# Optimization experiments

Measured on AMD Instinct MI355X. Metric: run time of the kernel, lower is better.

The kernel has to match this reference:

```python
import jax, jax.numpy as jnp
import numpy as np

N_NODES = 200000
N_EDGES = 3200000
N_GRAPHS = 2000
N_MAX = 256   # max nodes per graph for dense batching (mean ~100)
K = 30        # SortAggregation k


def setup_inputs() -> dict:
    key = jax.random.key(0)
    ks = jax.random.split(key, 12)
    x = jax.random.normal(ks[0], (N_NODES, 128), jnp.float32)
    edge_index = jax.random.randint(ks[1], (2, N_EDGES), 0, N_NODES, dtype=jnp.int32)
    batch = jnp.sort(jax.random.randint(ks[2], (N_NODES,), 0, N_GRAPHS, dtype=jnp.int32))
    def lin(k, i, o):
        return (jax.random.normal(k, (i, o), jnp.float32) / np.sqrt(i)).astype(jnp.float32)
    return {
        'x': x, 'edge_index': edge_index, 'batch': batch,
        'W1': lin(ks[3], 128, 32), 'b1': jnp.zeros(32, jnp.float32),
        'W2': lin(ks[4], 32, 32),  'b2': jnp.zeros(32, jnp.float32),
        'W3': lin(ks[5], 32, 32),  'b3': jnp.zeros(32, jnp.float32),
        'W4': lin(ks[6], 32, 1),   'b4': jnp.zeros(1, jnp.float32),
        'cw5': (jax.random.normal(ks[7], (16, 1, 97), jnp.float32) / np.sqrt(97)).astype(jnp.float32),
        'cb5': jnp.zeros(16, jnp.float32),
        'cw6': (jax.random.normal(ks[8], (32, 16, 5), jnp.float32) / np.sqrt(80)).astype(jnp.float32),
        'cb6': jnp.zeros(32, jnp.float32),
        'fw1': lin(ks[9], 352, 128), 'fb1': jnp.zeros(128, jnp.float32),
        'fw2': lin(ks[10], 128, 10), 'fb2': jnp.zeros(10, jnp.float32),
    }


def _gcn_conv(h, W, b, src, dst, emask):
    # PyG GCNConv: remove self-loops handled via emask (weight 0), then add
    # self-loops weight 1; symmetric normalization D^{-1/2}(A+I)D^{-1/2} X W + b
    deg = jax.ops.segment_sum(emask, dst, num_segments=N_NODES) + 1.0  # + self loop
    dis = jax.lax.rsqrt(deg)  # deg >= 1 always, no inf
    norm = dis[src] * dis[dst] * emask  # [E]
    hw = h @ W                          # [N, out]
    agg = jax.ops.segment_sum(hw[src] * norm[:, None], dst, num_segments=N_NODES)
    agg = agg + hw * (dis * dis)[:, None]  # self-loop message
    return agg + b


def _sort_pool(x, batch):
    # PyG SortAggregation(k): dense-batch with fill = min-1, sort each graph by
    # last feature channel (descending), keep top-k rows, zero out padding, flatten.
    N, D = x.shape
    ones = jnp.ones((N,), jnp.int32)
    counts = jax.ops.segment_sum(ones, batch, num_segments=N_GRAPHS)
    offsets = jnp.concatenate([jnp.zeros((1,), jnp.int32), jnp.cumsum(counts)[:-1]])
    pos = jnp.arange(N, dtype=jnp.int32) - offsets[batch]  # batch is sorted
    fill = x.min() - 1.0
    dense = jnp.full((N_GRAPHS, N_MAX, D), fill, x.dtype).at[batch, pos].set(x)
    perm = jnp.argsort(-dense[:, :, -1], axis=1)            # descending by last channel
    dense = jnp.take_along_axis(dense, perm[:, :, None], axis=1)[:, :K]  # [G, K, D]
    dense = jnp.where(dense == fill, 0.0, dense)
    return dense.reshape(N_GRAPHS, K * D)


def _conv1d(x, w, b, stride):
    y = jax.lax.conv_general_dilated(x, w, window_strides=(stride,), padding='VALID',
                                     dimension_numbers=('NCH', 'OIH', 'NCH'))
    return y + b[None, :, None]


def reference(x, edge_index, batch, W1, b1, W2, b2, W3, b3, W4, b4,
              cw5, cb5, cw6, cb6, fw1, fb1, fw2, fb2):
    src, dst = edge_index[0], edge_index[1]
    emask = (src != dst).astype(x.dtype)  # remove_self_loops

    x1 = jnp.tanh(_gcn_conv(x,  W1, b1, src, dst, emask))
    x2 = jnp.tanh(_gcn_conv(x1, W2, b2, src, dst, emask))
    x3 = jnp.tanh(_gcn_conv(x2, W3, b3, src, dst, emask))
    x4 = jnp.tanh(_gcn_conv(x3, W4, b4, src, dst, emask))
    h = jnp.concatenate([x1, x2, x3, x4], axis=-1)  # [N, 97]

    p = _sort_pool(h, batch)                 # [G, 30*97]
    p = p[:, None, :]                        # [G, 1, 2910]
    p = jax.nn.relu(_conv1d(p, cw5, cb5, 97))  # [G, 16, 30]
    G = p.shape[0]
    p = p.reshape(G, 16, 15, 2).max(axis=-1)   # MaxPool1d(2,2) -> [G, 16, 15]
    p = jax.nn.relu(_conv1d(p, cw6, cb6, 1))   # [G, 32, 11]
    p = p.reshape(G, -1)                       # [G, 352]
    out = jax.nn.relu(p @ fw1 + fb1)           # dropout is identity at inference
    return jax.nn.log_softmax(out @ fw2 + fb2, axis=-1)
```

## Files before the change

### kernel.cpp

```cpp
#include <hip/hip_runtime.h>

#define N_NODESC 200000
#define N_EDGESC 3200000
#define N_GRAPHSC 2000
#define NMAXG 256
#define TOPK 30
#define DCAT 97
#define POOLW (TOPK*DCAT)
#define BUCKW 512
#define NBUCK ((N_NODESC+BUCKW-1)/BUCKW)
#define CAP 10240
#define PCHUNK 4096
#define NPBLK ((N_EDGESC+PCHUNK-1)/PCHUNK)

typedef int  iv4 __attribute__((ext_vector_type(4)));
typedef float fv4 __attribute__((ext_vector_type(4)));

__global__ __launch_bounds__(256) void k_binit(int* __restrict__ bcur){
  int i = blockIdx.x*256 + threadIdx.x;
  if (i < NBUCK) bcur[i] = i*CAP;
}

__global__ __launch_bounds__(256) void k_part(const int* __restrict__ src, const int* __restrict__ dst,
                                              int* __restrict__ bcur, unsigned* __restrict__ pairbuf){
  __shared__ int hcnt[NBUCK];
  __shared__ int hbase[NBUCK];
  int blk = blockIdx.x, t = threadIdx.x;
  int e0 = blk*PCHUNK;
  int e1 = e0 + PCHUNK; if (e1 > N_EDGESC) e1 = N_EDGESC;
  for (int i=t;i<NBUCK;i+=256) hcnt[i]=0;
  unsigned pk[16]; unsigned meta[16];
  __syncthreads();
  #pragma unroll
  for (int i=0;i<4;i++){
    int e = e0 + i*1024 + t*4;
    if (e < e1){
      iv4 d4 = __builtin_nontemporal_load((const iv4*)(dst+e));
      iv4 s4 = __builtin_nontemporal_load((const iv4*)(src+e));
      #pragma unroll
      for (int k=0;k<4;k++){
        int d = (k==0)?d4.x:(k==1)?d4.y:(k==2)?d4.z:d4.w;
        int s = (k==0)?s4.x:(k==1)?s4.y:(k==2)?s4.z:s4.w;
        if (s!=d){
          int bk = d>>9;
          int pl = atomicAdd(&hcnt[bk],1);
          pk[i*4+k]   = ((unsigned)(d&511)<<18)|(unsigned)s;
          meta[i*4+k] = ((unsigned)bk<<13)|(unsigned)pl;
        } else meta[i*4+k] = 0xFFFFFFFFu;
      }
    } else {
      #pragma unroll
      for (int k=0;k<4;k++) meta[i*4+k] = 0xFFFFFFFFu;
    }
  }
  __syncthreads();
  for (int i=t;i<NBUCK;i+=256){
    int c = hcnt[i];
    hbase[i] = c ? atomicAdd(&bcur[i],c) : 0;
  }
  __syncthreads();
  #pragma unroll
  for (int k=0;k<16;k++){
    unsigned m = meta[k];
    if (m != 0xFFFFFFFFu){
      int bk = (int)(m>>13);
      int pos = hbase[bk] + (int)(m & 0x1FFFu);
      if (pos < (bk+1)*CAP) pairbuf[pos] = pk[k];
    }
  }
}

__global__ __launch_bounds__(512) void k_bsort(const unsigned* __restrict__ pairbuf, const int* __restrict__ bcur,
                                               int* __restrict__ degc, int* __restrict__ offs,
                                               float* __restrict__ dis, int* __restrict__ csr){
  __shared__ int lcsr[CAP];
  __shared__ int lcnt[512];
  __shared__ int lofs[512];
  __shared__ int lcur[512];
  __shared__ int red[512];
  int b = blockIdx.x, t = threadIdx.x;
  int cnt_b = bcur[b] - b*CAP; if (cnt_b > CAP) cnt_b = CAP;
  int pv = 0;
  if (t < b){ int c = bcur[t]-t*CAP; if (c>CAP) c=CAP; pv = c; }
  red[t]=pv; __syncthreads();
  for (int off=256;off>0;off>>=1){ if (t<off) red[t]+=red[t+off]; __syncthreads(); }
  int base = red[0];
  const unsigned* pb = pairbuf + (size_t)b*CAP;
  lcnt[t]=0; __syncthreads();
  for (int i=t;i<cnt_b;i+=512) atomicAdd(&lcnt[pb[i]>>18],1);
  __syncthreads();
  lofs[t]=lcnt[t]; __syncthreads();
  for (int off=1;off<512;off<<=1){
    int u = (t>=off)? lofs[t-off] : 0;
    __syncthreads();
    lofs[t]+=u;
    __syncthreads();
  }
  int excl = lofs[t]-lcnt[t];
  int node = b*BUCKW + t;
  if (node < N_NODESC){
    degc[node] = lcnt[t];
    offs[node] = base + excl;
    dis[node]  = rsqrtf((float)lcnt[t] + 1.0f);
  }
  lcur[t]=excl;
  __syncthreads();
  for (int i=t;i<cnt_b;i+=512){
    unsigned v = pb[i];
    int p = atomicAdd(&lcur[v>>18],1);
    lcsr[p] = (int)(v & 0x3FFFFu);
  }
  __syncthreads();
  for (int i=t;i<cnt_b;i+=512) csr[base+i]=lcsr[i];
}

__global__ void k_bhist(const int* __restrict__ batch, int* __restrict__ gcount){
  int i = blockIdx.x*256 + threadIdx.x;
  if (i < N_NODESC) atomicAdd(&gcount[batch[i]],1);
}

__global__ __launch_bounds__(1024) void k_gscan(const int* __restrict__ gcount, int* __restrict__ goff){
  __shared__ int sm[1024];
  int t=threadIdx.x;
  int i0=2*t, i1=2*t+1;
  int v0 = (i0<N_GRAPHSC)? gcount[i0]:0;
  int v1 = (i1<N_GRAPHSC)? gcount[i1]:0;
  int s = v0+v1;
  sm[t]=s; __syncthreads();
  for (int off=1;off<1024;off<<=1){
    int u=(t>=off)? sm[t-off]:0;
    __syncthreads();
    sm[t]+=u;
    __syncthreads();
  }
  int excl = sm[t]-s;
  if (i0<N_GRAPHSC) goff[i0]=excl;
  if (i1<N_GRAPHSC) goff[i1]=excl+v0;
}

template<int KIN>
__global__ __launch_bounds__(256) void k_mm(const float* __restrict__ X, const float* __restrict__ W,
                                            const float* __restrict__ dis, float* __restrict__ out){
  __shared__ float xs[256*33];
  int r0 = blockIdx.x*256;
  int t = threadIdx.x;
  int r = r0 + t;
  float acc[32];
  #pragma unroll
  for (int f=0;f<32;f++) acc[f]=0.f;
  for (int kc=0; kc<KIN; kc+=32){
    __syncthreads();
    #pragma unroll
    for (int it=0; it<8; it++){
      int idx = it*256 + t;
      int row = idx>>3, c4 = idx&7;
      int gr = r0 + row;
      fv4 v = {0.f,0.f,0.f,0.f};
      if (gr < N_NODESC) v = __builtin_nontemporal_load((const fv4*)(X + (size_t)gr*KIN + kc + c4*4));
      int bofs = row*33 + c4*4;
      xs[bofs]=v.x; xs[bofs+1]=v.y; xs[bofs+2]=v.z; xs[bofs+3]=v.w;
    }
    __syncthreads();
    const float* w0 = W + kc*32;
    const float* xrow = xs + t*33;
    #pragma unroll
    for (int k=0;k<32;k++){
      float xv = xrow[k];
      #pragma unroll
      for (int f=0;f<32;f++) acc[f] = fmaf(xv, w0[k*32+f], acc[f]);
    }
  }
  if (r >= N_NODESC) return;
  float d = dis[r];
  float4* op = (float4*)(out + (size_t)r*32);
  #pragma unroll
  for (int f4=0;f4<8;f4++)
    op[f4] = make_float4(acc[4*f4]*d, acc[4*f4+1]*d, acc[4*f4+2]*d, acc[4*f4+3]*d);
}

__global__ void k_mm4(const float* __restrict__ X, const float* __restrict__ W, const float* __restrict__ dis, float* __restrict__ out){
  int r = blockIdx.x*256+threadIdx.x;
  if (r>=N_NODESC) return;
  const float4* xr = (const float4*)(X + (size_t)r*32);
  float acc=0.f;
  #pragma unroll
  for (int k4=0;k4<8;k4++){
    float4 xv = xr[k4];
    acc = fmaf(xv.x, W[k4*4+0], acc);
    acc = fmaf(xv.y, W[k4*4+1], acc);
    acc = fmaf(xv.z, W[k4*4+2], acc);
    acc = fmaf(xv.w, W[k4*4+3], acc);
  }
  out[r]=acc*dis[r];
}

__global__ __launch_bounds__(256) void k_agg(const float* __restrict__ hws, const int* __restrict__ csr,
                      const int* __restrict__ off, const int* __restrict__ cnt,
                      const float* __restrict__ dis, const float* __restrict__ bias,
                      float* __restrict__ out){
  int t = blockIdx.x*256 + threadIdx.x;
  int n = t>>5;
  if (n>=N_NODESC) return;
  int f = t&31;
  int beg = off[n], c = cnt[n];
  float a0=0.f,a1=0.f,a2=0.f,a3=0.f,a4=0.f,a5=0.f,a6=0.f,a7=0.f;
  for (int base=0; base<c; base+=32){
    int m = c-base; if (m>32) m=32;
    int idx = (f<m)? csr[beg+base+f] : 0;
    int j=0;
    for (; j+8<=m; j+=8){
      int s0=__shfl(idx,j,32),   s1=__shfl(idx,j+1,32),
          s2=__shfl(idx,j+2,32), s3=__shfl(idx,j+3,32),
          s4=__shfl(idx,j+4,32), s5=__shfl(idx,j+5,32),
          s6=__shfl(idx,j+6,32), s7=__shfl(idx,j+7,32);
      float v0=hws[(size_t)s0*32+f];
      float v1=hws[(size_t)s1*32+f];
      float v2=hws[(size_t)s2*32+f];
      float v3=hws[(size_t)s3*32+f];
      float v4=hws[(size_t)s4*32+f];
      float v5=hws[(size_t)s5*32+f];
      float v6=hws[(size_t)s6*32+f];
      float v7=hws[(size_t)s7*32+f];
      a0+=v0; a1+=v1; a2+=v2; a3+=v3; a4+=v4; a5+=v5; a6+=v6; a7+=v7;
    }
    for (; j+4<=m; j+=4){
      int s0=__shfl(idx,j,32), s1=__shfl(idx,j+1,32),
          s2=__shfl(idx,j+2,32), s3=__shfl(idx,j+3,32);
      float v0=hws[(size_t)s0*32+f];
      float v1=hws[(size_t)s1*32+f];
      float v2=hws[(size_t)s2*32+f];
      float v3=hws[(size_t)s3*32+f];
      a0+=v0; a1+=v1; a2+=v2; a3+=v3;
    }
    for (; j<m; j++){
      int s0=__shfl(idx,j,32);
      a0 += hws[(size_t)s0*32+f];
    }
  }
  float dn = dis[n];
  float sum = ((a0+a1)+(a2+a3)) + ((a4+a5)+(a6+a7));
  float v = dn*(sum+hws[(size_t)n*32+f]) + bias[f];
  out[(size_t)n*32+f] = tanhf(v);
}

__global__ void k_agg4(const float* __restrict__ hws4, const int* __restrict__ csr,
                       const int* __restrict__ off, const int* __restrict__ cnt,
                       const float* __restrict__ dis, const float* __restrict__ b4,
                       float* __restrict__ x4){
  int n = blockIdx.x*256+threadIdx.x;
  if (n>=N_NODESC) return;
  int beg=off[n], c=cnt[n];
  float a0=0.f,a1=0.f,a2=0.f,a3=0.f,a4=0.f,a5=0.f,a6=0.f,a7=0.f;
  int e=0;
  for (; e+8<=c; e+=8){
    int s0=csr[beg+e],   s1=csr[beg+e+1], s2=csr[beg+e+2], s3=csr[beg+e+3];
    int s4=csr[beg+e+4], s5=csr[beg+e+5], s6=csr[beg+e+6], s7=csr[beg+e+7];
    a0+=hws4[s0]; a1+=hws4[s1]; a2+=hws4[s2]; a3+=hws4[s3];
    a4+=hws4[s4]; a5+=hws4[s5]; a6+=hws4[s6]; a7+=hws4[s7];
  }
  for (; e<c; e++) a0+=hws4[csr[beg+e]];
  float dn=dis[n];
  float sum = ((a0+a1)+(a2+a3)) + ((a4+a5)+(a6+a7));
  x4[n] = tanhf(dn*(sum+hws4[n]) + b4[0]);
}

__global__ __launch_bounds__(256) void k_sortpool(const float* __restrict__ x1,const float* __restrict__ x2,const float* __restrict__ x3,const float* __restrict__ x4,
                           const int* __restrict__ gcount, const int* __restrict__ goff, float* __restrict__ pool){
  __shared__ float vals[NMAXG];
  __shared__ int sel[TOPK];
  int g = blockIdx.x;
  int start = goff[g];
  int cntg = gcount[g]; if (cntg>NMAXG) cntg=NMAXG;
  int t = threadIdx.x;
  float v = 0.f;
  if (t<cntg) v = x4[start+t];
  vals[t] = v;
  __syncthreads();
  if (t<cntg){
    int rank=0;
    for (int j=0;j<cntg;j++){
      float vj=vals[j];
      rank += (vj>v) || (vj==v && j<t);
    }
    if (rank<TOPK) sel[rank]=t;
  }
  __syncthreads();
  int nsel = cntg<TOPK?cntg:TOPK;
  float* pg = pool + (size_t)g*POOLW;
  for (int idx=t; idx<POOLW; idx+=256){
    int r = idx/DCAT, c = idx - r*DCAT;
    float val=0.f;
    if (r<nsel){
      int node = start + sel[r];
      if (c<32) val = x1[(size_t)node*32+c];
      else if (c<64) val = x2[(size_t)node*32+(c-32)];
      else if (c<96) val = x3[(size_t)node*32+(c-64)];
      else val = x4[node];
    }
    pg[idx]=val;
  }
}

__global__ __launch_bounds__(128) void k_head(const float* __restrict__ pool,
                       const float* __restrict__ cw5, const float* __restrict__ cb5,
                       const float* __restrict__ cw6, const float* __restrict__ cb6,
                       const float* __restrict__ fw1, const float* __restrict__ fb1,
                       const float* __restrict__ fw2, const float* __restrict__ fb2,
                       float* __restrict__ out){
  __shared__ float P[POOLW];
  __shared__ float o5[16*30];
  __shared__ float m[16*15];
  __shared__ float o6[32*11];
  __shared__ float o1[128];
  __shared__ float logits[10];
  int g=blockIdx.x, t=threadIdx.x;
  const float* pg = pool + (size_t)g*POOLW;
  for (int i=t;i<POOLW;i+=128) P[i]=pg[i];
  __syncthreads();
  for (int i=t;i<480;i+=128){
    int o=i/30, k=i-o*30;
    float acc=cb5[o];
    const float* w=cw5+o*97;
    const float* p=P+k*97;
    for(int c=0;c<97;c++) acc = fmaf(p[c], w[c], acc);
    o5[o*30+k]=fmaxf(acc,0.f);
  }
  __syncthreads();
  for (int i=t;i<240;i+=128){
    int o=i/15,k=i-o*15;
    m[i]=fmaxf(o5[o*30+2*k], o5[o*30+2*k+1]);
  }
  __syncthreads();
  for (int i=t;i<352;i+=128){
    int o2=i/11, k=i-o2*11;
    float acc=cb6[o2];
    const float* w=cw6+o2*80;
    #pragma unroll
    for(int ii=0;ii<16;ii++)
      #pragma unroll
      for(int r=0;r<5;r++)
        acc = fmaf(m[ii*15+k+r], w[ii*5+r], acc);
    o6[o2*11+k]=fmaxf(acc,0.f);
  }
  __syncthreads();
  {
    float acc=fb1[t];
    for(int i=0;i<352;i++) acc = fmaf(o6[i], fw1[i*128+t], acc);
    o1[t]=fmaxf(acc,0.f);
  }
  __syncthreads();
  if (t<10){
    float acc=fb2[t];
    for(int j=0;j<128;j++) acc = fmaf(o1[j], fw2[j*10+t], acc);
    logits[t]=acc;
  }
  __syncthreads();
  if (t==0){
    float mx=logits[0];
    for(int c=1;c<10;c++) mx=fmaxf(mx,logits[c]);
    float s=0.f;
    for(int c=0;c<10;c++) s+=expf(logits[c]-mx);
    float lse=logf(s)+mx;
    for(int c=0;c<10;c++) out[(size_t)g*10+c]=logits[c]-lse;
  }
}

extern "C" void kernel_launch(void* const* d_in, const int* in_sizes, int n_in,
                              void* d_out, int out_size, void* d_ws, size_t ws_size,
                              hipStream_t stream){
  const float* x    = (const float*)d_in[0];
  const int*   ei   = (const int*)d_in[1];
  const int*   batch= (const int*)d_in[2];
  const float* W1=(const float*)d_in[3]; const float* b1=(const float*)d_in[4];
  const float* W2=(const float*)d_in[5]; const float* b2=(const float*)d_in[6];
  const float* W3=(const float*)d_in[7]; const float* b3=(const float*)d_in[8];
  const float* W4=(const float*)d_in[9]; const float* b4=(const float*)d_in[10];
  const float* cw5=(const float*)d_in[11]; const float* cb5=(const float*)d_in[12];
  const float* cw6=(const float*)d_in[13]; const float* cb6=(const float*)d_in[14];
  const float* fw1=(const float*)d_in[15]; const float* fb1=(const float*)d_in[16];
  const float* fw2=(const float*)d_in[17]; const float* fb2=(const float*)d_in[18];
  float* out=(float*)d_out;
  const int* src = ei;
  const int* dst = ei + N_EDGESC;

  char* ws=(char*)d_ws;
  size_t o=0;
  auto alloc=[&](size_t nbytes)->char*{ char* p=ws+o; o += (nbytes+255)&~(size_t)255; return p; };
  float* dis    = (float*)alloc((size_t)N_NODESC*4);
  int*   offs   = (int*)alloc((size_t)N_NODESC*4);
  int*   degc   = (int*)alloc((size_t)N_NODESC*4);
  int*   bcur   = (int*)alloc((size_t)NBUCK*4);
  int*   gcount = (int*)alloc((size_t)N_GRAPHSC*4);
  int*   goff   = (int*)alloc((size_t)N_GRAPHSC*4);
  unsigned* pairbuf = (unsigned*)alloc((size_t)NBUCK*CAP*4);
  int*   csr    = (int*)alloc((size_t)N_EDGESC*4);
  float* x1 = (float*)alloc((size_t)N_NODESC*32*4);
  float* x2 = (float*)alloc((size_t)N_NODESC*32*4);
  float* x3 = (float*)alloc((size_t)N_NODESC*32*4);
  float* x4 = (float*)alloc((size_t)N_NODESC*4);
  float* hw = (float*)alloc((size_t)N_NODESC*32*4);
  float* pool = hw;

  (void)hipMemsetAsync(gcount, 0, (size_t)N_GRAPHSC*4, stream);

  int gN = (N_NODESC+255)/256;

  k_binit<<<(NBUCK+255)/256,256,0,stream>>>(bcur);
  k_part<<<NPBLK,256,0,stream>>>(src,dst,bcur,pairbuf);
  k_bsort<<<NBUCK,512,0,stream>>>(pairbuf,bcur,degc,offs,dis,csr);

  k_bhist<<<gN,256,0,stream>>>(batch,gcount);
  k_gscan<<<1,1024,0,stream>>>(gcount,goff);

  int gMM=(N_NODESC+7)/8;
  k_mm<128><<<gN,256,0,stream>>>(x, W1, dis, hw);
  k_agg<<<gMM,256,0,stream>>>(hw,csr,offs,degc,dis,b1,x1);
  k_mm<32><<<gN,256,0,stream>>>(x1, W2, dis, hw);
  k_agg<<<gMM,256,0,stream>>>(hw,csr,offs,degc,dis,b2,x2);
  k_mm<32><<<gN,256,0,stream>>>(x2, W3, dis, hw);
  k_agg<<<gMM,256,0,stream>>>(hw,csr,offs,degc,dis,b3,x3);
  k_mm4<<<gN,256,0,stream>>>(x3, W4, dis, hw);
  k_agg4<<<gN,256,0,stream>>>(hw,csr,offs,degc,dis,b4,x4);

  k_sortpool<<<N_GRAPHSC,256,0,stream>>>(x1,x2,x3,x4,gcount,goff,pool);
  k_head<<<N_GRAPHSC,128,0,stream>>>(pool,cw5,cb5,cw6,cb6,fw1,fb1,fw2,fb2,out);
}
```

Measured before the change: 507.2 us.

## Fuse next-layer GCN weight matmul into the aggregation kernel epilogue

Each aggregation kernel now applies tanh and then immediately multiplies the resulting 32-wide row by the next layer's weight matrix, using wave shuffles and a shared-memory copy of W. This removes the separate k_mm<32> and k_mm4 launches and their re-read of x1/x2/x3 from global memory. It ping-pongs between two hw buffers and adds a reduction path that writes the scalar hw4 for the last layer. The cost is a 1024-float shared-memory load per block and 32 shuffles plus FMAs per thread in the aggregation kernels, which may lower occupancy.

Result: no change. 516.8 us (+1.9%).

```diff
diff --git a/kernel.cpp b/kernel.cpp
--- a/kernel.cpp
+++ b/kernel.cpp
@@ -178,30 +178,19 @@
     op[f4] = make_float4(acc[4*f4]*d, acc[4*f4+1]*d, acc[4*f4+2]*d, acc[4*f4+3]*d);
 }
 
-__global__ void k_mm4(const float* __restrict__ X, const float* __restrict__ W, const float* __restrict__ dis, float* __restrict__ out){
-  int r = blockIdx.x*256+threadIdx.x;
-  if (r>=N_NODESC) return;
-  const float4* xr = (const float4*)(X + (size_t)r*32);
-  float acc=0.f;
-  #pragma unroll
-  for (int k4=0;k4<8;k4++){
-    float4 xv = xr[k4];
-    acc = fmaf(xv.x, W[k4*4+0], acc);
-    acc = fmaf(xv.y, W[k4*4+1], acc);
-    acc = fmaf(xv.z, W[k4*4+2], acc);
-    acc = fmaf(xv.w, W[k4*4+3], acc);
-  }
-  out[r]=acc*dis[r];
-}
-
-__global__ __launch_bounds__(256) void k_agg(const float* __restrict__ hws, const int* __restrict__ csr,
+__global__ __launch_bounds__(256) void k_aggF32(const float* __restrict__ hws, const int* __restrict__ csr,
                       const int* __restrict__ off, const int* __restrict__ cnt,
                       const float* __restrict__ dis, const float* __restrict__ bias,
-                      float* __restrict__ out){
-  int t = blockIdx.x*256 + threadIdx.x;
-  int n = t>>5;
+                      const float* __restrict__ Wn,
+                      float* __restrict__ xout, float* __restrict__ hwn){
+  __shared__ float Ws[1024];
+  int t = threadIdx.x;
+  for (int i=t;i<1024;i+=256) Ws[i]=Wn[i];
+  __syncthreads();
+  int gt = blockIdx.x*256 + t;
+  int n = gt>>5;
   if (n>=N_NODESC) return;
-  int f = t&31;
+  int f = gt&31;
   int beg = off[n], c = cnt[n];
   float a0=0.f,a1=0.f,a2=0.f,a3=0.f,a4=0.f,a5=0.f,a6=0.f,a7=0.f;
   for (int base=0; base<c; base+=32){
@@ -239,8 +228,73 @@
   }
   float dn = dis[n];
   float sum = ((a0+a1)+(a2+a3)) + ((a4+a5)+(a6+a7));
-  float v = dn*(sum+hws[(size_t)n*32+f]) + bias[f];
-  out[(size_t)n*32+f] = tanhf(v);
+  float xv = tanhf(dn*(sum+hws[(size_t)n*32+f]) + bias[f]);
+  xout[(size_t)n*32+f] = xv;
+  float acc = 0.f;
+  #pragma unroll
+  for (int k=0;k<32;k++){
+    float vk = __shfl(xv, k, 32);
+    acc = fmaf(vk, Ws[k*32+f], acc);
+  }
+  hwn[(size_t)n*32+f] = acc*dn;
+}
+
+__global__ __launch_bounds__(256) void k_aggF1(const float* __restrict__ hws, const int* __restrict__ csr,
+                      const int* __restrict__ off, const int* __restrict__ cnt,
+                      const float* __restrict__ dis, const float* __restrict__ bias,
+                      const float* __restrict__ W4,
+                      float* __restrict__ xout, float* __restrict__ hw4){
+  __shared__ float Ws[32];
+  int t = threadIdx.x;
+  if (t<32) Ws[t]=W4[t];
+  __syncthreads();
+  int gt = blockIdx.x*256 + t;
+  int n = gt>>5;
+  if (n>=N_NODESC) return;
+  int f = gt&31;
+  int beg = off[n], c = cnt[n];
+  float a0=0.f,a1=0.f,a2=0.f,a3=0.f,a4=0.f,a5=0.f,a6=0.f,a7=0.f;
+  for (int base=0; base<c; base+=32){
+    int m = c-base; if (m>32) m=32;
+    int idx = (f<m)? csr[beg+base+f] : 0;
+    int j=0;
+    for (; j+8<=m; j+=8){
+      int s0=__shfl(idx,j,32),   s1=__shfl(idx,j+1,32),
+          s2=__shfl(idx,j+2,32), s3=__shfl(idx,j+3,32),
+          s4=__shfl(idx,j+4,32), s5=__shfl(idx,j+5,32),
+          s6=__shfl(idx,j+6,32), s7=__shfl(idx,j+7,32);
+      float v0=hws[(size_t)s0*32+f];
+      float v1=hws[(size_t)s1*32+f];
+      float v2=hws[(size_t)s2*32+f];
+      float v3=hws[(size_t)s3*32+f];
+      float v4=hws[(size_t)s4*32+f];
+      float v5=hws[(size_t)s5*32+f];
+      float v6=hws[(size_t)s6*32+f];
+      float v7=hws[(size_t)s7*32+f];
+      a0+=v0; a1+=v1; a2+=v2; a3+=v3; a4+=v4; a5+=v5; a6+=v6; a7+=v7;
+    }
+    for (; j+4<=m; j+=4){
+      int s0=__shfl(idx,j,32), s1=__shfl(idx,j+1,32),
+          s2=__shfl(idx,j+2,32), s3=__shfl(idx,j+3,32);
+      float v0=hws[(size_t)s0*32+f];
+      float v1=hws[(size_t)s1*32+f];
+      float v2=hws[(size_t)s2*32+f];
+      float v3=hws[(size_t)s3*32+f];
+      a0+=v0; a1+=v1; a2+=v2; a3+=v3;
+    }
+    for (; j<m; j++){
+      int s0=__shfl(idx,j,32);
+      a0 += hws[(size_t)s0*32+f];
+    }
+  }
+  float dn = dis[n];
+  float sum = ((a0+a1)+(a2+a3)) + ((a4+a5)+(a6+a7));
+  float xv = tanhf(dn*(sum+hws[(size_t)n*32+f]) + bias[f]);
+  xout[(size_t)n*32+f] = xv;
+  float acc = xv*Ws[f];
+  #pragma unroll
+  for (int off2=16;off2>0;off2>>=1) acc += __shfl_xor(acc, off2, 32);
+  if (f==0) hw4[n] = acc*dn;
 }
 
 __global__ void k_agg4(const float* __restrict__ hws4, const int* __restrict__ csr,
@@ -398,8 +452,10 @@
   float* x2 = (float*)alloc((size_t)N_NODESC*32*4);
   float* x3 = (float*)alloc((size_t)N_NODESC*32*4);
   float* x4 = (float*)alloc((size_t)N_NODESC*4);
-  float* hw = (float*)alloc((size_t)N_NODESC*32*4);
-  float* pool = hw;
+  float* hwA = (float*)alloc((size_t)N_NODESC*32*4);
+  float* hwB = (float*)alloc((size_t)N_NODESC*32*4);
+  float* hw4 = (float*)alloc((size_t)N_NODESC*4);
+  float* pool = hwB;
 
   (void)hipMemsetAsync(gcount, 0, (size_t)N_GRAPHSC*4, stream);
 
@@ -413,14 +469,11 @@
   k_gscan<<<1,1024,0,stream>>>(gcount,goff);
 
   int gMM=(N_NODESC+7)/8;
-  k_mm<128><<<gN,256,0,stream>>>(x, W1, dis, hw);
-  k_agg<<<gMM,256,0,stream>>>(hw,csr,offs,degc,dis,b1,x1);
-  k_mm<32><<<gN,256,0,stream>>>(x1, W2, dis, hw);
-  k_agg<<<gMM,256,0,stream>>>(hw,csr,offs,degc,dis,b2,x2);
-  k_mm<32><<<gN,256,0,stream>>>(x2, W3, dis, hw);
-  k_agg<<<gMM,256,0,stream>>>(hw,csr,offs,degc,dis,b3,x3);
-  k_mm4<<<gN,256,0,stream>>>(x3, W4, dis, hw);
-  k_agg4<<<gN,256,0,stream>>>(hw,csr,offs,degc,dis,b4,x4);
+  k_mm<128><<<gN,256,0,stream>>>(x, W1, dis, hwA);
+  k_aggF32<<<gMM,256,0,stream>>>(hwA,csr,offs,degc,dis,b1,W2,x1,hwB);
+  k_aggF32<<<gMM,256,0,stream>>>(hwB,csr,offs,degc,dis,b2,W3,x2,hwA);
+  k_aggF1 <<<gMM,256,0,stream>>>(hwA,csr,offs,degc,dis,b3,W4,x3,hw4);
+  k_agg4  <<<gN,256,0,stream>>>(hw4,csr,offs,degc,dis,b4,x4);
 
   k_sortpool<<<N_GRAPHSC,256,0,stream>>>(x1,x2,x3,x4,gcount,goff,pool);
   k_head<<<N_GRAPHSC,128,0,stream>>>(pool,cw5,cb5,cw6,cb6,fw1,fb1,fw2,fb2,out);
```

## Fold bucket init, graph histogram and prefix scan into existing kernels

Applied to the files above, without the earlier changes.

Drops the separate bucket-init, batch-histogram and graph-scan launches. Bucket cursors now start at zero from one combined memset and the bucket base is added at use. The graph histogram runs inside the edge-partition kernel, which has NPBLK=782 blocks and so covers all 200000 nodes. Each sort-pool block recomputes its graph offset with a block-level reduction over preceding counts, which costs some redundant reads of gcount (up to 2000 ints per block) in exchange for three fewer launches.

After: 485.9 us. -4.2%, faster.

```diff
diff --git a/kernel.cpp b/kernel.cpp
--- a/kernel.cpp
+++ b/kernel.cpp
@@ -16,16 +16,14 @@
 typedef int  iv4 __attribute__((ext_vector_type(4)));
 typedef float fv4 __attribute__((ext_vector_type(4)));
 
-__global__ __launch_bounds__(256) void k_binit(int* __restrict__ bcur){
-  int i = blockIdx.x*256 + threadIdx.x;
-  if (i < NBUCK) bcur[i] = i*CAP;
-}
-
 __global__ __launch_bounds__(256) void k_part(const int* __restrict__ src, const int* __restrict__ dst,
+                                              const int* __restrict__ batch, int* __restrict__ gcount,
                                               int* __restrict__ bcur, unsigned* __restrict__ pairbuf){
   __shared__ int hcnt[NBUCK];
   __shared__ int hbase[NBUCK];
   int blk = blockIdx.x, t = threadIdx.x;
+  int nd = blk*256 + t;
+  if (nd < N_NODESC) atomicAdd(&gcount[batch[nd]],1);
   int e0 = blk*PCHUNK;
   int e1 = e0 + PCHUNK; if (e1 > N_EDGESC) e1 = N_EDGESC;
   for (int i=t;i<NBUCK;i+=256) hcnt[i]=0;
@@ -56,7 +54,7 @@
   __syncthreads();
   for (int i=t;i<NBUCK;i+=256){
     int c = hcnt[i];
-    hbase[i] = c ? atomicAdd(&bcur[i],c) : 0;
+    hbase[i] = c ? (i*CAP + atomicAdd(&bcur[i],c)) : 0;
   }
   __syncthreads();
   #pragma unroll
@@ -79,9 +77,9 @@
   __shared__ int lcur[512];
   __shared__ int red[512];
   int b = blockIdx.x, t = threadIdx.x;
-  int cnt_b = bcur[b] - b*CAP; if (cnt_b > CAP) cnt_b = CAP;
+  int cnt_b = bcur[b]; if (cnt_b > CAP) cnt_b = CAP;
   int pv = 0;
-  if (t < b){ int c = bcur[t]-t*CAP; if (c>CAP) c=CAP; pv = c; }
+  if (t < b){ int c = bcur[t]; if (c>CAP) c=CAP; pv = c; }
   red[t]=pv; __syncthreads();
   for (int off=256;off>0;off>>=1){ if (t<off) red[t]+=red[t+off]; __syncthreads(); }
   int base = red[0];
@@ -112,30 +110,6 @@
   }
   __syncthreads();
   for (int i=t;i<cnt_b;i+=512) csr[base+i]=lcsr[i];
-}
-
-__global__ void k_bhist(const int* __restrict__ batch, int* __restrict__ gcount){
-  int i = blockIdx.x*256 + threadIdx.x;
-  if (i < N_NODESC) atomicAdd(&gcount[batch[i]],1);
-}
-
-__global__ __launch_bounds__(1024) void k_gscan(const int* __restrict__ gcount, int* __restrict__ goff){
-  __shared__ int sm[1024];
-  int t=threadIdx.x;
-  int i0=2*t, i1=2*t+1;
-  int v0 = (i0<N_GRAPHSC)? gcount[i0]:0;
-  int v1 = (i1<N_GRAPHSC)? gcount[i1]:0;
-  int s = v0+v1;
-  sm[t]=s; __syncthreads();
-  for (int off=1;off<1024;off<<=1){
-    int u=(t>=off)? sm[t-off]:0;
-    __syncthreads();
-    sm[t]+=u;
-    __syncthreads();
-  }
-  int excl = sm[t]-s;
-  if (i0<N_GRAPHSC) goff[i0]=excl;
-  if (i1<N_GRAPHSC) goff[i1]=excl+v0;
 }
 
 template<int KIN>
@@ -265,13 +239,18 @@
 }
 
 __global__ __launch_bounds__(256) void k_sortpool(const float* __restrict__ x1,const float* __restrict__ x2,const float* __restrict__ x3,const float* __restrict__ x4,
-                           const int* __restrict__ gcount, const int* __restrict__ goff, float* __restrict__ pool){
+                           const int* __restrict__ gcount, float* __restrict__ pool){
   __shared__ float vals[NMAXG];
   __shared__ int sel[TOPK];
+  __shared__ int redsum[256];
   int g = blockIdx.x;
-  int start = goff[g];
+  int t = threadIdx.x;
+  int part = 0;
+  for (int i=t; i<g; i+=256) part += gcount[i];
+  redsum[t]=part; __syncthreads();
+  for (int off=128;off>0;off>>=1){ if (t<off) redsum[t]+=redsum[t+off]; __syncthreads(); }
+  int start = redsum[0];
   int cntg = gcount[g]; if (cntg>NMAXG) cntg=NMAXG;
-  int t = threadIdx.x;
   float v = 0.f;
   if (t<cntg) v = x4[start+t];
   vals[t] = v;
@@ -391,7 +370,6 @@
   int*   degc   = (int*)alloc((size_t)N_NODESC*4);
   int*   bcur   = (int*)alloc((size_t)NBUCK*4);
   int*   gcount = (int*)alloc((size_t)N_GRAPHSC*4);
-  int*   goff   = (int*)alloc((size_t)N_GRAPHSC*4);
   unsigned* pairbuf = (unsigned*)alloc((size_t)NBUCK*CAP*4);
   int*   csr    = (int*)alloc((size_t)N_EDGESC*4);
   float* x1 = (float*)alloc((size_t)N_NODESC*32*4);
@@ -401,16 +379,13 @@
   float* hw = (float*)alloc((size_t)N_NODESC*32*4);
   float* pool = hw;
 
-  (void)hipMemsetAsync(gcount, 0, (size_t)N_GRAPHSC*4, stream);
+  size_t mset = (((size_t)NBUCK*4+255)&~(size_t)255) + (size_t)N_GRAPHSC*4;
+  (void)hipMemsetAsync(bcur, 0, mset, stream);
 
   int gN = (N_NODESC+255)/256;
 
-  k_binit<<<(NBUCK+255)/256,256,0,stream>>>(bcur);
-  k_part<<<NPBLK,256,0,stream>>>(src,dst,bcur,pairbuf);
+  k_part<<<NPBLK,256,0,stream>>>(src,dst,batch,gcount,bcur,pairbuf);
   k_bsort<<<NBUCK,512,0,stream>>>(pairbuf,bcur,degc,offs,dis,csr);
-
-  k_bhist<<<gN,256,0,stream>>>(batch,gcount);
-  k_gscan<<<1,1024,0,stream>>>(gcount,goff);
 
   int gMM=(N_NODESC+7)/8;
   k_mm<128><<<gN,256,0,stream>>>(x, W1, dis, hw);
@@ -422,6 +397,6 @@
   k_mm4<<<gN,256,0,stream>>>(x3, W4, dis, hw);
   k_agg4<<<gN,256,0,stream>>>(hw,csr,offs,degc,dis,b4,x4);
 
-  k_sortpool<<<N_GRAPHSC,256,0,stream>>>(x1,x2,x3,x4,gcount,goff,pool);
+  k_sortpool<<<N_GRAPHSC,256,0,stream>>>(x1,x2,x3,x4,gcount,pool);
   k_head<<<N_GRAPHSC,128,0,stream>>>(pool,cw5,cb5,cw6,cb6,fw1,fb1,fw2,fb2,out);
 }
```
